# Performance work log

Hardware: AMD Instinct MI355X
Metric: run time of the kernel (lower is better)

Reference implementation:

```python
import jax, jax.numpy as jnp
import numpy as np

PRED_STEPS = 5
NEG = 16
C = 256
B = 64
H = 16
W = 16
SKIP = 1
EPS = 1e-11


def setup_inputs() -> dict:
    key = jax.random.key(0)
    ks = jax.random.split(key, 3 + PRED_STEPS)
    inp = {
        "z": jax.random.normal(ks[0], (B, C, H, W), jnp.float32),
        "c": jax.random.normal(ks[1], (B, C, H, W), jnp.float32),
        "Wk": jax.random.normal(ks[2], (PRED_STEPS, C, C), jnp.float32) * 0.05,
    }
    for k in range(1, PRED_STEPS + 1):
        rows = (H - k - SKIP) * W * B
        inp[f"rand_idx_{k}"] = jax.random.randint(ks[2 + k], (rows * NEG,), 0, rows, dtype=jnp.int64 if jax.config.jax_enable_x64 else jnp.int32)
    return inp


def reference(z, c, Wk, rand_idx_1, rand_idx_2, rand_idx_3, rand_idx_4, rand_idx_5):
    idx_list = [rand_idx_1, rand_idx_2, rand_idx_3, rand_idx_4, rand_idx_5]
    total_loss = jnp.float32(0.0)
    patchwise_loss = jnp.zeros((B, H, W), jnp.float32)
    patchwise_count = jnp.zeros((H, W), jnp.float32)
    for k in range(1, PRED_STEPS + 1):
        off = k + SKIP
        Hk = H - off
        # 1x1 conv projection, permuted to [Hk, W, B, C]
        ztwk = jnp.einsum('oi,bihw->hwbo', Wk[k - 1], z[:, :, off:, :])
        # random-gather negatives: [Hk, W, B, NEG, C]
        flat = ztwk.reshape(Hk * W * B, C)
        ztwk_shuf = flat[idx_list[k - 1]].reshape(Hk, W, B, NEG, C)
        # context: [Hk, W, B, C]
        ctx = jnp.transpose(c[:, :, :Hk, :], (2, 3, 0, 1))
        # scoring
        main = jnp.einsum('hwbc,hwbc->hwb', ctx, ztwk)[..., None]        # [Hk,W,B,1]
        negs = jnp.einsum('hwbc,hwbnc->hwbn', ctx, ztwk_shuf)            # [Hk,W,B,NEG]
        logits = jnp.concatenate([main, negs], axis=-1)                  # [Hk,W,B,1+NEG]
        log_fk = jnp.transpose(logits, (2, 3, 0, 1))                     # [B,1+NEG,Hk,W]
        sm = jax.nn.softmax(log_fk, axis=1)
        stu_loss = -jnp.log(sm[:, 0, :, :] + EPS)                        # [B,Hk,W]
        total_loss = total_loss + stu_loss.mean()
        patchwise_loss = patchwise_loss.at[:, off:, :].add(stu_loss)
        patchwise_loss = patchwise_loss.at[:, :H - off, :].add(stu_loss)
        ones = jnp.ones((Hk, W), jnp.float32)
        patchwise_count = patchwise_count.at[off:, :].add(ones)
        patchwise_count = patchwise_count.at[:H - off, :].add(ones)
    total_loss = total_loss / PRED_STEPS
    return (total_loss, patchwise_loss, patchwise_count)
```

## Files before the change

### kernel.cpp

```cpp
#include <hip/hip_runtime.h>
#include <hip/hip_bf16.h>
#include <math.h>

#define NEG_ 16
#define PRED_ 5
#define EPS_ 1e-11f
#define LDW 18
#define GSTR 272
#define ASTR 72

typedef __attribute__((ext_vector_type(8))) short bf16x8;
typedef __attribute__((ext_vector_type(4))) float f32x4;

static __device__ __forceinline__ unsigned short f2bu(float f) {
  __hip_bfloat16 h = __float2bfloat16(f);
  return *(unsigned short*)&h;
}


__global__ __launch_bounds__(256) void prep_all(
    const float* __restrict__ z, const float* __restrict__ c,
    const float* __restrict__ Wk,
    unsigned short* __restrict__ Zp, unsigned short* __restrict__ Cb,
    unsigned short* __restrict__ Wb, float* __restrict__ out) {
  __shared__ float tile[32][65];
  const int t = threadIdx.x;
  if (blockIdx.x == 0 && blockIdx.y == 0 && blockIdx.z == 0 && t == 0)
    out[0] = 0.f;
  if (blockIdx.y == 7) {
    int ib = blockIdx.z * 256 + blockIdx.x;
    if (ib < 320) {
      const int k = ib >> 6, tl = ib & 63;
      const int r0 = (tl >> 3) * 32, c0g = (tl & 7) * 32;
      const int tx = t & 31, ty = t >> 5;
#pragma unroll
      for (int r = 0; r < 32; r += 8)
        tile[ty + r][tx] = Wk[k * 65536 + (r0 + ty + r) * 256 + c0g + tx];
      __syncthreads();
#pragma unroll
      for (int r = 0; r < 32; r += 8)
        Wb[k * 65536 + (c0g + ty + r) * 256 + r0 + tx] = f2bu(tile[tx][ty + r]);
    }
    return;
  }
  const float* in = blockIdx.z ? c : z;
  unsigned short* out2 = blockIdx.z ? Cb : Zp;
  const int p0 = blockIdx.x * 64;
  const int q0 = blockIdx.y * 32 + (blockIdx.z ? 0 : 32);
  const int tx = t & 31, ty = t >> 5;
#pragma unroll
  for (int r = 0; r < 64; r += 8)
    tile[tx][ty + r] = in[(size_t)(p0 + ty + r) * 256 + q0 + tx];
  __syncthreads();
  const int pp = t & 63, wq = t >> 6;
#pragma unroll
  for (int r = 0; r < 32; r += 4)
    out2[(size_t)(q0 + wq + r) * 16384 + p0 + pp] = f2bu(tile[wq + r][pp]);
}

__global__ __launch_bounds__(256) void gemm_all(
    const unsigned short* __restrict__ Cb, const unsigned short* __restrict__ Wb,
    unsigned short* __restrict__ Cw) {
  const int kk = blockIdx.z;
  const int Mk = (14 - kk) * 1024;
  const int m0b = blockIdx.y * 128;
  if (m0b >= Mk) return;
  const unsigned short* A = Cb;
  const unsigned short* Wm = Wb + (size_t)kk * 65536;
  unsigned short* Y = Cw + (size_t)kk * 14336 * 256;
  __shared__ unsigned short As[128 * ASTR];
  __shared__ unsigned short Bs[128 * ASTR];
  const int t = threadIdx.x;
  const int wid = t >> 6, lane = t & 63;
  const int wm = wid >> 1, wn = wid & 1;
  const int l15 = lane & 15, quad = lane >> 4;
  const int n0 = blockIdx.x * 128;
  const int srow = t >> 1, shalf = t & 1;
  const unsigned short* ga = A + (size_t)(m0b + srow) * 256 + shalf * 32;
  const unsigned short* gb = Wm + (size_t)(n0 + srow) * 256 + shalf * 32;
  unsigned short* wa = As + srow * ASTR + shalf * 32;
  unsigned short* wb = Bs + srow * ASTR + shalf * 32;
  f32x4 acc[4][4] = {};
  bf16x8 ra[4], rb[4];
#pragma unroll
  for (int cs = 0; cs < 4; ++cs) {
    ra[cs] = *(const bf16x8*)(ga + cs * 8);
    rb[cs] = *(const bf16x8*)(gb + cs * 8);
  }
#pragma unroll
  for (int ki = 0; ki < 4; ++ki) {
    __syncthreads();
#pragma unroll
    for (int cs = 0; cs < 4; ++cs) {
      *(bf16x8*)(wa + cs * 8) = ra[cs];
      *(bf16x8*)(wb + cs * 8) = rb[cs];
    }
    __syncthreads();
    if (ki < 3) {
      const int k1 = (ki + 1) * 64;
#pragma unroll
      for (int cs = 0; cs < 4; ++cs) {
        ra[cs] = *(const bf16x8*)(ga + k1 + cs * 8);
        rb[cs] = *(const bf16x8*)(gb + k1 + cs * 8);
      }
    }
#pragma unroll
    for (int ks = 0; ks < 2; ++ks) {
      bf16x8 af[4], bf[4];
#pragma unroll
      for (int tm = 0; tm < 4; ++tm)
        af[tm] = *(const bf16x8*)(As + (wm * 64 + tm * 16 + l15) * ASTR + ks * 32 + quad * 8);
#pragma unroll
      for (int tn = 0; tn < 4; ++tn)
        bf[tn] = *(const bf16x8*)(Bs + (wn * 64 + tn * 16 + l15) * ASTR + ks * 32 + quad * 8);
#pragma unroll
      for (int tm = 0; tm < 4; ++tm)
#pragma unroll
        for (int tn = 0; tn < 4; ++tn)
          acc[tm][tn] = __builtin_amdgcn_mfma_f32_16x16x32_bf16(
              af[tm], bf[tn], acc[tm][tn], 0, 0, 0);
    }
  }
#pragma unroll
  for (int tm = 0; tm < 4; ++tm)
#pragma unroll
    for (int tn = 0; tn < 4; ++tn)
#pragma unroll
      for (int r = 0; r < 4; ++r)
        Y[(size_t)(m0b + wm * 64 + tm * 16 + quad * 4 + r) * 256 +
          n0 + wn * 64 + tn * 16 + l15] = f2bu(acc[tm][tn][r]);
}

__global__ __launch_bounds__(256) void score_all(
    const unsigned short* __restrict__ Cw, const unsigned short* __restrict__ Zp,
    const int* __restrict__ r1, const int* __restrict__ r2,
    const int* __restrict__ r3, const int* __restrict__ r4,
    const int* __restrict__ r5, float* __restrict__ Lk) {
  __shared__ __align__(16) unsigned short gbuf[4][16 * GSTR];
  __shared__ float L[16 * LDW];
  const int wv = threadIdx.x >> 6, lane = threadIdx.x & 63;
  const int gid = blockIdx.x;
  int kk, base;
  if (gid < 896)       { kk = 0; base = 0; }
  else if (gid < 1728) { kk = 1; base = 896; }
  else if (gid < 2496) { kk = 2; base = 1728; }
  else if (gid < 3200) { kk = 3; base = 2496; }
  else                 { kk = 4; base = 3200; }
  const int Mk = (14 - kk) * 1024;
  const int m0 = (gid - base) * 16;
  const int* ridx = kk == 0 ? r1 : kk == 1 ? r2 : kk == 2 ? r3 : kk == 3 ? r4 : r5;
  const unsigned short* Yc = Cw + (size_t)kk * 14336 * 256;
  const unsigned short* Z  = Zp + (size_t)(kk + 2) * 1024 * 256;
  const int l15 = lane & 15, quad = lane >> 4;
  const int half = lane >> 5, ch = lane & 31;
  unsigned short* mybuf = gbuf[wv];

  auto gather = [&](const unsigned short* src, int ivv, bf16x8* dst) {
#pragma unroll
    for (int j = 0; j < 8; ++j) {
      int rlo = __shfl(ivv, 2 * j);
      int rhi = __shfl(ivv, 2 * j + 1);
      int row = half ? rhi : rlo;
      dst[j] = *(const bf16x8*)(src + (size_t)row * 256 + ch * 8);
    }
  };
  auto stage = [&](const bf16x8* g) {
#pragma unroll
    for (int j2 = 0; j2 < 8; ++j2)
      *(bf16x8*)(mybuf + (2 * j2 + half) * GSTR + ch * 8) = g[j2];
  };

  const int c0 = (wv == 0) ? 0 : (4 * wv + 1);
  const int nc = (wv == 0) ? 5 : 4;
  int iv[5];
#pragma unroll
  for (int j = 0; j < 5; ++j) {
    if (j < nc) {
      const int c = c0 + j;
      if (c == 0) iv[j] = m0 + l15;
      else {
        int idx = ridx[(m0 + (c - 1)) * NEG_ + l15];
        iv[j] = idx < 0 ? 0 : (idx >= Mk ? Mk - 1 : idx);
      }
    } else iv[j] = 0;
  }

  bf16x8 g[8];
  gather(Yc, m0 + l15, g);
  bf16x8 bA[8], bB[8];
  gather(Z, iv[0], bA);
  if (nc > 1) gather(Z, iv[1], bB);
  stage(g);
  bf16x8 af[8];
#pragma unroll
  for (int tv = 0; tv < 8; ++tv)
    af[tv] = *(const bf16x8*)(mybuf + l15 * GSTR + quad * 8 + tv * 32);

#pragma unroll
  for (int j = 0; j < 5; ++j) {
    if (j < nc) {
      if (j & 1) {
        stage(bB);
        if (j + 2 < nc) gather(Z, iv[j + 2], bB);
      } else {
        stage(bA);
        if (j + 2 < nc) gather(Z, iv[j + 2], bA);
      }
      f32x4 acc = {};
#pragma unroll
      for (int tv = 0; tv < 8; ++tv) {
        bf16x8 bfv = *(const bf16x8*)(mybuf + l15 * GSTR + quad * 8 + tv * 32);
        acc = __builtin_amdgcn_mfma_f32_16x16x32_bf16(af[tv], bfv, acc, 0, 0, 0);
      }
      const int c = c0 + j;
      if (c == 0) {
#pragma unroll
        for (int r = 0; r < 4; ++r)
          if (l15 == quad * 4 + r) L[(quad * 4 + r) * LDW] = acc[r];
      } else {
        const int i = c - 1;
        if (quad == (i >> 2)) L[i * LDW + 1 + l15] = acc[i & 3];
      }
    }
  }
  __syncthreads();
  if (threadIdx.x < 16) {
    float mainv = L[threadIdx.x * LDW];
    float mx = mainv;
    float nv[NEG_];
#pragma unroll
    for (int n = 0; n < NEG_; ++n) {
      nv[n] = L[threadIdx.x * LDW + 1 + n];
      mx = fmaxf(mx, nv[n]);
    }
    float num = __expf(mainv - mx);
    float se = num;
#pragma unroll
    for (int n = 0; n < NEG_; ++n) se += __expf(nv[n] - mx);
    Lk[kk * 14336 + m0 + threadIdx.x] = -logf(num / se + EPS_);
  }
}

__global__ __launch_bounds__(256) void finalize_pl(
    const float* __restrict__ Lk, float* __restrict__ out) {
  if (blockIdx.x < 64) {
    int idx = blockIdx.x * 256 + threadIdx.x;
    int b = idx >> 8, h = (idx >> 4) & 15, w = idx & 15;
    float v = 0.f;
#pragma unroll
    for (int kk = 0; kk < PRED_; ++kk) {
      int off = kk + 2;
      if (h >= off)      v += Lk[kk * 14336 + ((h - off) * 16 + w) * 64 + b];
      if (h <= 15 - off) v += Lk[kk * 14336 + (h * 16 + w) * 64 + b];
    }
    out[1 + idx] = v;
    if (idx < 256) {
      int hh = idx >> 4;
      float cnt = 0.f;
#pragma unroll
      for (int off = 2; off <= 6; ++off)
        cnt += (hh >= off ? 1.f : 0.f) + (hh <= 15 - off ? 1.f : 0.f);
      out[1 + 16384 + idx] = cnt;
    }
  } else {
    __shared__ float red[4];
    const int cb = blockIdx.x - 64;
    const int kk = cb < 14 ? 0 : cb < 27 ? 1 : cb < 39 ? 2 : cb < 50 ? 3 : 4;
    const int s0 = kk == 0 ? 0 : kk == 1 ? 14 : kk == 2 ? 27 : kk == 3 ? 39 : 50;
    const float scale = 1.0f / (5120.0f * (float)(14 - kk));
    const int e = (cb - s0) * 1024 + threadIdx.x * 4;
    float4 v = *(const float4*)&Lk[kk * 14336 + e];
    float local = (v.x + v.y + v.z + v.w) * scale;
#pragma unroll
    for (int s = 32; s; s >>= 1) local += __shfl_down(local, s);
    if ((threadIdx.x & 63) == 0) red[threadIdx.x >> 6] = local;
    __syncthreads();
    if (threadIdx.x == 0)
      atomicAdd(out, red[0] + red[1] + red[2] + red[3]);
  }
}

extern "C" void kernel_launch(void* const* d_in, const int* in_sizes, int n_in,
                              void* d_out, int out_size, void* d_ws, size_t ws_size,
                              hipStream_t stream) {
  const float* z  = (const float*)d_in[0];
  const float* c  = (const float*)d_in[1];
  const float* Wk = (const float*)d_in[2];
  float* out = (float*)d_out;
  char* wsb = (char*)d_ws;
  unsigned short* Zp = (unsigned short*)(wsb);
  unsigned short* Cb = (unsigned short*)(wsb + 8388608);
  unsigned short* Wb = (unsigned short*)(wsb + 16777216);
  unsigned short* Cw = (unsigned short*)(wsb + 17432576);
  float*          Lk = (float*)(wsb + 54132736);

  prep_all<<<dim3(256, 8, 2), 256, 0, stream>>>(z, c, Wk, Zp, Cb, Wb, out);
  gemm_all<<<dim3(2, 112, PRED_), 256, 0, stream>>>(Cb, Wb, Cw);
  score_all<<<3840, 256, 0, stream>>>(
      Cw, Zp, (const int*)d_in[3], (const int*)d_in[4], (const int*)d_in[5],
      (const int*)d_in[6], (const int*)d_in[7], Lk);
  finalize_pl<<<124, 256, 0, stream>>>(Lk, out);
}
```

Before: 150.4 us.

## Split score gather into two row-range passes with merged online softmax

```diff
diff --git a/kernel.cpp b/kernel.cpp
--- a/kernel.cpp
+++ b/kernel.cpp
@@ -8,6 +8,8 @@
 #define LDW 18
 #define GSTR 272
 #define ASTR 72
+#define SPLIT_ROW 8192
+#define NEGINF_ -1e30f
 
 typedef __attribute__((ext_vector_type(8))) short bf16x8;
 typedef __attribute__((ext_vector_type(4))) float f32x4;
@@ -131,11 +133,13 @@
           n0 + wn * 64 + tn * 16 + l15] = f2bu(acc[tm][tn][r]);
 }
 
-__global__ __launch_bounds__(256) void score_all(
+template <int PASS>
+__global__ __launch_bounds__(256) void score_pass(
     const unsigned short* __restrict__ Cw, const unsigned short* __restrict__ Zp,
     const int* __restrict__ r1, const int* __restrict__ r2,
     const int* __restrict__ r3, const int* __restrict__ r4,
-    const int* __restrict__ r5, float* __restrict__ Lk) {
+    const int* __restrict__ r5, float* __restrict__ statsA,
+    float* __restrict__ Lk) {
   __shared__ __align__(16) unsigned short gbuf[4][16 * GSTR];
   __shared__ float L[16 * LDW];
   const int wv = threadIdx.x >> 6, lane = threadIdx.x & 63;
@@ -148,9 +152,10 @@
   else                 { kk = 4; base = 3200; }
   const int Mk = (14 - kk) * 1024;
   const int m0 = (gid - base) * 16;
+  const int base_off = (kk + 2) * 1024;
   const int* ridx = kk == 0 ? r1 : kk == 1 ? r2 : kk == 2 ? r3 : kk == 3 ? r4 : r5;
   const unsigned short* Yc = Cw + (size_t)kk * 14336 * 256;
-  const unsigned short* Z  = Zp + (size_t)(kk + 2) * 1024 * 256;
+  const unsigned short* Z  = Zp + (size_t)base_off * 256;
   const int l15 = lane & 15, quad = lane >> 4;
   const int half = lane >> 5, ch = lane & 31;
   unsigned short* mybuf = gbuf[wv];
@@ -172,39 +177,55 @@
 
   const int c0 = (wv == 0) ? 0 : (4 * wv + 1);
   const int nc = (wv == 0) ? 5 : 4;
-  int iv[5];
+  int ivp[5];
+  bool pe[5];
+  const int dummyB = SPLIT_ROW - base_off;
 #pragma unroll
   for (int j = 0; j < 5; ++j) {
+    ivp[j] = 0; pe[j] = false;
     if (j < nc) {
       const int c = c0 + j;
-      if (c == 0) iv[j] = m0 + l15;
+      int rel;
+      if (c == 0) rel = m0 + l15;
       else {
         int idx = ridx[(m0 + (c - 1)) * NEG_ + l15];
-        iv[j] = idx < 0 ? 0 : (idx >= Mk ? Mk - 1 : idx);
-      }
-    } else iv[j] = 0;
-  }
-
-  bf16x8 g[8];
-  gather(Yc, m0 + l15, g);
+        rel = idx < 0 ? 0 : (idx >= Mk ? Mk - 1 : idx);
+      }
+      const bool inA = (rel + base_off) < SPLIT_ROW;
+      pe[j] = (PASS == 0) ? inA : !inA;
+      ivp[j] = pe[j] ? rel : (PASS == 0 ? 0 : dummyB);
+    }
+  }
+
+  bf16x8 af[8];
+  {
+    bf16x8 g[8];
+#pragma unroll
+    for (int j = 0; j < 8; ++j) {
+      int row = m0 + (half ? 2 * j + 1 : 2 * j) - 0;
+      g[j] = __builtin_nontemporal_load(
+          (const bf16x8*)(Yc + (size_t)(m0 + 2 * j + half) * 256 + ch * 8));
+      (void)row;
+    }
+    stage(g);
+#pragma unroll
+    for (int tv = 0; tv < 8; ++tv)
+      af[tv] = *(const bf16x8*)(mybuf + l15 * GSTR + quad * 8 + tv * 32);
+  }
+
   bf16x8 bA[8], bB[8];
-  gather(Z, iv[0], bA);
-  if (nc > 1) gather(Z, iv[1], bB);
-  stage(g);
-  bf16x8 af[8];
-#pragma unroll
-  for (int tv = 0; tv < 8; ++tv)
-    af[tv] = *(const bf16x8*)(mybuf + l15 * GSTR + quad * 8 + tv * 32);
+  gather(Z, ivp[0], bA);
+  if (nc > 1) gather(Z, ivp[1], bB);
 
 #pragma unroll
   for (int j = 0; j < 5; ++j) {
     if (j < nc) {
       if (j & 1) {
         stage(bB);
-        if (j + 2 < nc) gather(Z, iv[j + 2], bB);
+        if (j + 2 < nc) gather(Z, ivp[j + 2], bB);
       } else {
         stage(bA);
-        if (j + 2 < nc) gather(Z, iv[j + 2], bA);
+        if (j + 2 < nc) gather(Z, ivp[j + 2], bA);
       }
       f32x4 acc = {};
 #pragma unroll
@@ -216,28 +237,47 @@
       if (c == 0) {
 #pragma unroll
         for (int r = 0; r < 4; ++r)
-          if (l15 == quad * 4 + r) L[(quad * 4 + r) * LDW] = acc[r];
+          if (l15 == quad * 4 + r) L[(quad * 4 + r) * LDW] = pe[j] ? acc[r] : NEGINF_;
       } else {
         const int i = c - 1;
-        if (quad == (i >> 2)) L[i * LDW + 1 + l15] = acc[i & 3];
+        if (quad == (i >> 2)) L[i * LDW + 1 + l15] = pe[j] ? acc[i & 3] : NEGINF_;
       }
     }
   }
   __syncthreads();
   if (threadIdx.x < 16) {
-    float mainv = L[threadIdx.x * LDW];
+    const int t = threadIdx.x;
+    float mainv = L[t * LDW];
     float mx = mainv;
     float nv[NEG_];
 #pragma unroll
     for (int n = 0; n < NEG_; ++n) {
-      nv[n] = L[threadIdx.x * LDW + 1 + n];
+      nv[n] = L[t * LDW + 1 + n];
       mx = fmaxf(mx, nv[n]);
     }
-    float num = __expf(mainv - mx);
-    float se = num;
-#pragma unroll
-    for (int n = 0; n < NEG_; ++n) se += __expf(nv[n] - mx);
-    Lk[kk * 14336 + m0 + threadIdx.x] = -logf(num / se + EPS_);
+    float s;
+    if (mx < -1e29f) {
+      s = 0.f;
+    } else {
+      s = __expf(mainv - mx);
+#pragma unroll
+      for (int n = 0; n < NEG_; ++n) s += __expf(nv[n] - mx);
+    }
+    const int rowi = kk * 14336 + m0 + t;
+    if (PASS == 0) {
+      statsA[rowi * 3 + 0] = mx;
+      statsA[rowi * 3 + 1] = s;
+      statsA[rowi * 3 + 2] = mainv;
+    } else {
+      const float mA = statsA[rowi * 3 + 0];
+      const float sA = statsA[rowi * 3 + 1];
+      const float mvA = statsA[rowi * 3 + 2];
+      const bool mainB = (m0 + t + base_off) >= SPLIT_ROW;
+      const float mv = mainB ? mainv : mvA;
+      const float m = fmaxf(mA, mx);
+      const float se = sA * __expf(mA - m) + s * __expf(mx - m);
+      Lk[rowi] = -logf(__expf(mv - m) / se + EPS_);
+    }
   }
 }
 
@@ -288,6 +328,7 @@
   const float* Wk = (const float*)d_in[2];
   float* out = (float*)d_out;
   char* wsb = (char*)d_ws;
+  float*          SA = (float*)(wsb);
   unsigned short* Zp = (unsigned short*)(wsb);
   unsigned short* Cb = (unsigned short*)(wsb + 8388608);
   unsigned short* Wb = (unsigned short*)(wsb + 16777216);
@@ -296,8 +337,11 @@
 
   prep_all<<<dim3(256, 8, 2), 256, 0, stream>>>(z, c, Wk, Zp, Cb, Wb, out);
   gemm_all<<<dim3(2, 112, PRED_), 256, 0, stream>>>(Cb, Wb, Cw);
-  score_all<<<3840, 256, 0, stream>>>(
+  score_pass<0><<<3840, 256, 0, stream>>>(
       Cw, Zp, (const int*)d_in[3], (const int*)d_in[4], (const int*)d_in[5],
-      (const int*)d_in[6], (const int*)d_in[7], Lk);
+      (const int*)d_in[6], (const int*)d_in[7], SA, Lk);
+  score_pass<1><<<3840, 256, 0, stream>>>(
+      Cw, Zp, (const int*)d_in[3], (const int*)d_in[4], (const int*)d_in[5],
+      (const int*)d_in[6], (const int*)d_in[7], SA, Lk);
   finalize_pl<<<124, 256, 0, stream>>>(Lk, out);
 }
```

Result: slower. 180.9 us (+20.3%).
